# Performance work log

Measured on AMD Instinct MI355X. Metric: run time of the kernel, lower is better.

The kernel has to match this reference:

```python
import jax, jax.numpy as jnp
import numpy as np

N = 131072; E = 1048576; B = 1024
FIN = 128; H = 128; K = 30; C1 = 16; KERN = 5
D = 3 * H                      # 384 = hidden*num_layers
POOL_LEN = (K - KERN + 1) // 2 # 13
EPS = 1e-5


def setup_inputs() -> dict:
    key = jax.random.key(0)
    ks = jax.random.split(key, 12)
    w = lambda k, shape, s=0.05: (jax.random.normal(k, shape, jnp.float32) * s)
    z = jax.random.randint(ks[0], (N,), 0, FIN, dtype=jnp.int32)
    edge_index = jax.random.randint(ks[1], (2, E), 0, N, dtype=jnp.int32)
    batch = jnp.sort(jax.random.randint(ks[2], (N,), 0, B, dtype=jnp.int32))
    return dict(
        z=z, edge_index=edge_index, batch=batch,
        W0=w(ks[3], (FIN, H)), b0=jnp.zeros((H,), jnp.float32),
        W1=w(ks[4], (H, H)),   b1=jnp.zeros((H,), jnp.float32),
        W2=w(ks[5], (H, H)),   b2=jnp.zeros((H,), jnp.float32),
        Wc1=w(ks[6], (C1, D)), bc1=jnp.zeros((C1,), jnp.float32),
        Wc2=w(ks[7], (2 * C1, C1, KERN)), bc2=jnp.zeros((2 * C1,), jnp.float32),
        g1=jnp.ones((C1,), jnp.float32),  be1=jnp.zeros((C1,), jnp.float32),
        g2=jnp.ones((2 * C1,), jnp.float32), be2=jnp.zeros((2 * C1,), jnp.float32),
        Wl1=w(ks[8], (128, 2 * C1 * POOL_LEN)), bl1=jnp.zeros((128,), jnp.float32),
        Wl2=w(ks[9], (1, 128)), bl2=jnp.zeros((1,), jnp.float32),
        rm1=jnp.zeros((C1,), jnp.float32), rv1=jnp.ones((C1,), jnp.float32),
        rm2=jnp.zeros((2 * C1,), jnp.float32), rv2=jnp.ones((2 * C1,), jnp.float32),
    )


def _bn(h, g, be, rm, rv):
    # eval-mode BatchNorm1d over channel axis 1 of [B, C, L]
    scale = (g * jax.lax.rsqrt(rv + EPS))[None, :, None]
    return (h - rm[None, :, None]) * scale + be[None, :, None]


def _forward(z, edge_index, batch, W0, b0, W1, b1, W2, b2, Wc1, bc1, Wc2, bc2,
             g1, be1, g2, be2, Wl1, bl1, Wl2, bl2, rm1, rv1, rm2, rv2):
    # --- GCN normalization with self-loops (PyG gcn_norm) ---
    loops = jnp.arange(N)
    row = jnp.concatenate([edge_index[0], loops])  # source
    col = jnp.concatenate([edge_index[1], loops])  # target (aggregation)
    deg = jax.ops.segment_sum(jnp.ones(E + N, jnp.float32), col, num_segments=N)
    dis = jax.lax.rsqrt(deg)  # deg >= 1 thanks to self-loops
    norm = dis[row] * dis[col]

    def gcn(x, W, b):
        msg = (x @ W)[row] * norm[:, None]              # [E+N, H]
        return jax.ops.segment_sum(msg, col, num_segments=N) + b

    x = jax.nn.one_hot(z, FIN, dtype=jnp.float32)       # [N, FIN]
    xs = []
    for W, b in ((W0, b0), (W1, b1), (W2, b2)):
        x = jnp.tanh(gcn(x, W, b))
        xs.append(x)
    x = jnp.concatenate(xs, axis=-1)                    # [N, D]

    # --- global_sort_pool: per graph, sort by last channel desc, keep top-k, zero-pad ---
    order = jnp.lexsort((-x[:, -1], batch))             # batch asc, last-channel desc
    xb, bs = x[order], batch[order]
    counts = jax.ops.segment_sum(jnp.ones(N, jnp.int32), batch, num_segments=B)
    starts = jnp.cumsum(counts) - counts
    rank = jnp.arange(N) - starts[bs]                   # within-graph rank
    dest = jnp.where(rank < K, rank, K)                 # overflow bucket at K
    pooled = jnp.zeros((B, K + 1, D), jnp.float32).at[bs, dest].set(xb)[:, :K]  # [B,K,D]

    # --- conv1d_1 (kernel=stride=D) == dense over the D channels of each kept node ---
    h = jnp.einsum('bkd,cd->bck', pooled, Wc1) + bc1[None, :, None]  # [B,C1,K]
    h = _bn(jax.nn.relu(h), g1, be1, rm1, rv1)
    # --- conv1d_2 ---
    h = jax.lax.conv_general_dilated(h, Wc2, (1,), 'VALID',
                                     dimension_numbers=('NCH', 'OIH', 'NCH'))
    h = h + bc2[None, :, None]                          # [B,2C1,K-KERN+1]
    h = _bn(jax.nn.relu(h), g2, be2, rm2, rv2)
    # --- maxpool(2,2), flatten, dense head (dropout is identity in eval) ---
    h = h.reshape(B, 2 * C1, POOL_LEN, 2).max(-1)
    h = jax.nn.relu(h.reshape(B, -1) @ Wl1.T + bl1)
    return (h @ Wl2.T + bl2).reshape(-1)                # [B]


def reference(z, edge_index, batch, W0, b0, W1, b1, W2, b2, Wc1, bc1, Wc2, bc2,
              g1, be1, g2, be2, Wl1, bl1, Wl2, bl2, rm1, rv1, rm2, rv2):
    return _forward(z, edge_index, batch, W0, b0, W1, b1, W2, b2, Wc1, bc1, Wc2, bc2,
                    g1, be1, g2, be2, Wl1, bl1, Wl2, bl2, rm1, rv1, rm2, rv2)
```

## Files before the change

kernel.cpp:

```cpp
#include <hip/hip_runtime.h>
#include <math.h>

constexpr int HD = 128;
constexpr int DD = 384;
constexpr int KK = 30;
constexpr int C1N = 16;
constexpr int C2N = 32;
constexpr int KERN5 = 5;
constexpr int CONVL = 26;
constexpr int PL = 13;
constexpr int FLAT = 416;

__global__ void deg_kernel(const int* __restrict__ col, int* __restrict__ cnt, int E) {
  int e = blockIdx.x * blockDim.x + threadIdx.x;
  if (e < E) atomicAdd(&cnt[col[e]], 1);
}

__global__ void scan1_kernel(const int* __restrict__ cnt, int* __restrict__ bsum, int N) {
  __shared__ int red[256];
  int t = threadIdx.x, b = blockIdx.x;
  int base = b * 1024 + t * 4;
  int s = 0;
#pragma unroll
  for (int j = 0; j < 4; ++j) { int idx = base + j; if (idx < N) s += cnt[idx]; }
  red[t] = s;
  __syncthreads();
  for (int o = 128; o > 0; o >>= 1) { if (t < o) red[t] += red[t + o]; __syncthreads(); }
  if (t == 0) bsum[b] = red[0];
}

__global__ void scan2_kernel(int* __restrict__ bsum, int nb) {
  __shared__ int s[1024];
  int t = threadIdx.x;
  int v = (t < nb) ? bsum[t] : 0;
  s[t] = v;
  __syncthreads();
  for (int o = 1; o < 1024; o <<= 1) {
    int u = (t >= o) ? s[t - o] : 0;
    __syncthreads();
    s[t] += u;
    __syncthreads();
  }
  if (t < nb) bsum[t] = s[t] - v;
}

__global__ void scan3_kernel(const int* __restrict__ cnt, const int* __restrict__ bsum,
                             int* __restrict__ offsets, int N) {
  __shared__ int red[256];
  int t = threadIdx.x, b = blockIdx.x;
  int base = b * 1024 + t * 4;
  int v[4]; int s = 0;
#pragma unroll
  for (int j = 0; j < 4; ++j) { int idx = base + j; v[j] = (idx < N) ? cnt[idx] : 0; s += v[j]; }
  red[t] = s;
  __syncthreads();
  for (int o = 1; o < 256; o <<= 1) {
    int u = (t >= o) ? red[t - o] : 0;
    __syncthreads();
    red[t] += u;
    __syncthreads();
  }
  int run = bsum[b] + red[t] - s;
#pragma unroll
  for (int j = 0; j < 4; ++j) {
    int idx = base + j;
    if (idx < N) {
      offsets[idx] = run;
      run += v[j];
      if (idx == N - 1) offsets[N] = run;
    }
  }
}

__global__ void dis_kernel(const int* __restrict__ cnt, float* __restrict__ dis, int N) {
  int i = blockIdx.x * blockDim.x + threadIdx.x;
  if (i < N) dis[i] = 1.0f / sqrtf((float)(cnt[i] + 1));
}

__global__ void fill_kernel(const int* __restrict__ row, const int* __restrict__ col,
                            const int* __restrict__ offsets, int* __restrict__ cursor,
                            int* __restrict__ csr_src, int E) {
  int e = blockIdx.x * blockDim.x + threadIdx.x;
  if (e < E) {
    int c = col[e];
    int p = offsets[c] + atomicAdd(&cursor[c], 1);
    csr_src[p] = row[e];
  }
}

__global__ __launch_bounds__(256) void agg0_kernel(
    const int* __restrict__ z, const int* __restrict__ offsets,
    const int* __restrict__ csr_src, const float* __restrict__ dis,
    const float* __restrict__ W0, const float* __restrict__ b0,
    float* __restrict__ x1, int N) {
  int wid = (blockIdx.x * blockDim.x + threadIdx.x) >> 6;
  int lane = threadIdx.x & 63;
  if (wid >= N) return;
  int i = wid;
  int c0 = lane * 2;
  float di = dis[i];
  int beg = offsets[i], end = offsets[i + 1];
  float ax = 0.f, ay = 0.f;
  int e = beg;
  for (; e + 8 <= end; e += 8) {
    int s0 = csr_src[e],     s1 = csr_src[e + 1], s2 = csr_src[e + 2], s3 = csr_src[e + 3];
    int s4 = csr_src[e + 4], s5 = csr_src[e + 5], s6 = csr_src[e + 6], s7 = csr_src[e + 7];
    float w0 = dis[s0], w1 = dis[s1], w2 = dis[s2], w3 = dis[s3];
    float w4 = dis[s4], w5 = dis[s5], w6 = dis[s6], w7 = dis[s7];
    const float2 y0 = *(const float2*)(W0 + (size_t)z[s0] * HD + c0);
    const float2 y1 = *(const float2*)(W0 + (size_t)z[s1] * HD + c0);
    const float2 y2 = *(const float2*)(W0 + (size_t)z[s2] * HD + c0);
    const float2 y3 = *(const float2*)(W0 + (size_t)z[s3] * HD + c0);
    const float2 y4 = *(const float2*)(W0 + (size_t)z[s4] * HD + c0);
    const float2 y5 = *(const float2*)(W0 + (size_t)z[s5] * HD + c0);
    const float2 y6 = *(const float2*)(W0 + (size_t)z[s6] * HD + c0);
    const float2 y7 = *(const float2*)(W0 + (size_t)z[s7] * HD + c0);
    float axa = fmaf(w0, y0.x, fmaf(w1, y1.x, fmaf(w2, y2.x, w3 * y3.x)));
    float axb = fmaf(w4, y4.x, fmaf(w5, y5.x, fmaf(w6, y6.x, w7 * y7.x)));
    float aya = fmaf(w0, y0.y, fmaf(w1, y1.y, fmaf(w2, y2.y, w3 * y3.y)));
    float ayb = fmaf(w4, y4.y, fmaf(w5, y5.y, fmaf(w6, y6.y, w7 * y7.y)));
    ax += axa + axb;
    ay += aya + ayb;
  }
  for (; e + 4 <= end; e += 4) {
    int s0 = csr_src[e], s1 = csr_src[e + 1], s2 = csr_src[e + 2], s3 = csr_src[e + 3];
    float w0 = dis[s0], w1 = dis[s1], w2 = dis[s2], w3 = dis[s3];
    const float2 y0 = *(const float2*)(W0 + (size_t)z[s0] * HD + c0);
    const float2 y1 = *(const float2*)(W0 + (size_t)z[s1] * HD + c0);
    const float2 y2 = *(const float2*)(W0 + (size_t)z[s2] * HD + c0);
    const float2 y3 = *(const float2*)(W0 + (size_t)z[s3] * HD + c0);
    ax = fmaf(w0, y0.x, fmaf(w1, y1.x, fmaf(w2, y2.x, fmaf(w3, y3.x, ax))));
    ay = fmaf(w0, y0.y, fmaf(w1, y1.y, fmaf(w2, y2.y, fmaf(w3, y3.y, ay))));
  }
  for (; e < end; ++e) {
    int s = csr_src[e];
    float w = dis[s];
    const float2 ys = *(const float2*)(W0 + (size_t)z[s] * HD + c0);
    ax = fmaf(w, ys.x, ax);
    ay = fmaf(w, ys.y, ay);
  }
  const float2 yi = *(const float2*)(W0 + (size_t)z[i] * HD + c0);
  float inv = di * di;
  float ox = tanhf(di * ax + inv * yi.x + b0[c0]);
  float oy = tanhf(di * ay + inv * yi.y + b0[c0 + 1]);
  *(float2*)(x1 + (size_t)i * HD + c0) = make_float2(ox, oy);
}

__global__ __launch_bounds__(256) void agg_kernel(
    const float* __restrict__ x, const int* __restrict__ offsets,
    const int* __restrict__ csr_src, const float* __restrict__ dis,
    float* __restrict__ T, int N) {
  int wid = (blockIdx.x * blockDim.x + threadIdx.x) >> 6;
  int lane = threadIdx.x & 63;
  if (wid >= N) return;
  int i = wid;
  int c0 = lane * 2;
  float di = dis[i];
  int beg = offsets[i], end = offsets[i + 1];
  float ax = 0.f, ay = 0.f;
  int e = beg;
  for (; e + 8 <= end; e += 8) {
    int s0 = csr_src[e],     s1 = csr_src[e + 1], s2 = csr_src[e + 2], s3 = csr_src[e + 3];
    int s4 = csr_src[e + 4], s5 = csr_src[e + 5], s6 = csr_src[e + 6], s7 = csr_src[e + 7];
    float w0 = dis[s0], w1 = dis[s1], w2 = dis[s2], w3 = dis[s3];
    float w4 = dis[s4], w5 = dis[s5], w6 = dis[s6], w7 = dis[s7];
    const float2 y0 = *(const float2*)(x + (size_t)s0 * HD + c0);
    const float2 y1 = *(const float2*)(x + (size_t)s1 * HD + c0);
    const float2 y2 = *(const float2*)(x + (size_t)s2 * HD + c0);
    const float2 y3 = *(const float2*)(x + (size_t)s3 * HD + c0);
    const float2 y4 = *(const float2*)(x + (size_t)s4 * HD + c0);
    const float2 y5 = *(const float2*)(x + (size_t)s5 * HD + c0);
    const float2 y6 = *(const float2*)(x + (size_t)s6 * HD + c0);
    const float2 y7 = *(const float2*)(x + (size_t)s7 * HD + c0);
    float axa = fmaf(w0, y0.x, fmaf(w1, y1.x, fmaf(w2, y2.x, w3 * y3.x)));
    float axb = fmaf(w4, y4.x, fmaf(w5, y5.x, fmaf(w6, y6.x, w7 * y7.x)));
    float aya = fmaf(w0, y0.y, fmaf(w1, y1.y, fmaf(w2, y2.y, w3 * y3.y)));
    float ayb = fmaf(w4, y4.y, fmaf(w5, y5.y, fmaf(w6, y6.y, w7 * y7.y)));
    ax += axa + axb;
    ay += aya + ayb;
  }
  for (; e + 4 <= end; e += 4) {
    int s0 = csr_src[e], s1 = csr_src[e + 1], s2 = csr_src[e + 2], s3 = csr_src[e + 3];
    float w0 = dis[s0], w1 = dis[s1], w2 = dis[s2], w3 = dis[s3];
    const float2 y0 = *(const float2*)(x + (size_t)s0 * HD + c0);
    const float2 y1 = *(const float2*)(x + (size_t)s1 * HD + c0);
    const float2 y2 = *(const float2*)(x + (size_t)s2 * HD + c0);
    const float2 y3 = *(const float2*)(x + (size_t)s3 * HD + c0);
    ax = fmaf(w0, y0.x, fmaf(w1, y1.x, fmaf(w2, y2.x, fmaf(w3, y3.x, ax))));
    ay = fmaf(w0, y0.y, fmaf(w1, y1.y, fmaf(w2, y2.y, fmaf(w3, y3.y, ay))));
  }
  for (; e < end; ++e) {
    int s = csr_src[e];
    float w = dis[s];
    const float2 xs = *(const float2*)(x + (size_t)s * HD + c0);
    ax = fmaf(w, xs.x, ax);
    ay = fmaf(w, xs.y, ay);
  }
  const float2 xi = *(const float2*)(x + (size_t)i * HD + c0);
  float inv = di * di;
  float ox = di * ax + inv * xi.x;
  float oy = di * ay + inv * xi.y;
  *(float2*)(T + (size_t)i * HD + c0) = make_float2(ox, oy);
}

__global__ __launch_bounds__(256) void gemm_kernel(
    float* __restrict__ T, const float* __restrict__ W, const float* __restrict__ b, int N) {
  __shared__ float Xs[128][33];
  __shared__ float Ws[32][128];
  int t = threadIdx.x;
  int r0 = blockIdx.x * 128;
  int ty = t >> 4, tx = t & 15;
  int R0 = ty * 8;
  float acc[8][8];
#pragma unroll
  for (int a = 0; a < 8; ++a)
#pragma unroll
    for (int c = 0; c < 8; ++c) acc[a][c] = 0.f;

  for (int kb = 0; kb < 128; kb += 32) {
    __syncthreads();
    for (int l = t; l < 1024; l += 256) {
      int r = l >> 3, c4 = (l & 7) << 2;
      float4 v = *(const float4*)(T + (size_t)(r0 + r) * HD + kb + c4);
      Xs[r][c4] = v.x; Xs[r][c4 + 1] = v.y; Xs[r][c4 + 2] = v.z; Xs[r][c4 + 3] = v.w;
    }
    for (int l = t; l < 1024; l += 256) {
      int k = l >> 5, c4 = (l & 31) << 2;
      *(float4*)(&Ws[k][c4]) = *(const float4*)(W + (size_t)(kb + k) * HD + c4);
    }
    __syncthreads();
#pragma unroll
    for (int k = 0; k < 32; ++k) {
      float a[8];
#pragma unroll
      for (int ri = 0; ri < 8; ++ri) a[ri] = Xs[R0 + ri][k];
      float4 blo = *(const float4*)(&Ws[k][tx * 4]);
      float4 bhi = *(const float4*)(&Ws[k][64 + tx * 4]);
      float bb[8] = {blo.x, blo.y, blo.z, blo.w, bhi.x, bhi.y, bhi.z, bhi.w};
#pragma unroll
      for (int ri = 0; ri < 8; ++ri)
#pragma unroll
        for (int ci = 0; ci < 8; ++ci)
          acc[ri][ci] = fmaf(a[ri], bb[ci], acc[ri][ci]);
    }
  }
  float4 bl = *(const float4*)(b + tx * 4);
  float4 bh = *(const float4*)(b + 64 + tx * 4);
#pragma unroll
  for (int ri = 0; ri < 8; ++ri) {
    float4 o0 = make_float4(tanhf(acc[ri][0] + bl.x), tanhf(acc[ri][1] + bl.y),
                            tanhf(acc[ri][2] + bl.z), tanhf(acc[ri][3] + bl.w));
    float4 o1 = make_float4(tanhf(acc[ri][4] + bh.x), tanhf(acc[ri][5] + bh.y),
                            tanhf(acc[ri][6] + bh.z), tanhf(acc[ri][7] + bh.w));
    *(float4*)(T + (size_t)(r0 + R0 + ri) * HD + tx * 4) = o0;
    *(float4*)(T + (size_t)(r0 + R0 + ri) * HD + 64 + tx * 4) = o1;
  }
}

__global__ void gstart_kernel(const int* __restrict__ batch, int* __restrict__ gstart,
                              int N, int B) {
  int g = blockIdx.x * blockDim.x + threadIdx.x;
  if (g > B) return;
  int lo = 0, hi = N;
  while (lo < hi) { int mid = (lo + hi) >> 1; if (batch[mid] < g) lo = mid + 1; else hi = mid; }
  gstart[g] = lo;
}

__global__ __launch_bounds__(512) void head_kernel(
    const float* __restrict__ X1, const float* __restrict__ X2, const float* __restrict__ X3,
    const int* __restrict__ gstart,
    const float* __restrict__ Wc1, const float* __restrict__ bc1,
    const float* __restrict__ Wc2, const float* __restrict__ bc2,
    const float* __restrict__ g1, const float* __restrict__ be1,
    const float* __restrict__ g2, const float* __restrict__ be2,
    const float* __restrict__ rm1, const float* __restrict__ rv1,
    const float* __restrict__ rm2, const float* __restrict__ rv2,
    const float* __restrict__ Wl1, const float* __restrict__ bl1,
    const float* __restrict__ Wl2, const float* __restrict__ bl2,
    float* __restrict__ out) {
  constexpr int MAXC = 512;
  __shared__ float vals[MAXC];
  __shared__ int   sel[KK];
  __shared__ float ph[KK][385];
  __shared__ float h1b[C1N][KK + 1];
  float* h2b  = &ph[0][0];
  float* pp   = &ph[0][0] + 832;
  float* part = &ph[0][0] + 1248;
  float* l1v  = &ph[0][0] + 1760;

  int g = blockIdx.x, t = threadIdx.x;
  int start = gstart[g];
  int count = gstart[g + 1] - start;
  if (count > MAXC) count = MAXC;
  int kk = count < KK ? count : KK;

  for (int i = t; i < count; i += 512)
    vals[i] = X3[(size_t)(start + i) * HD + (HD - 1)];
  __syncthreads();
  if (t < count) {
    float vi = vals[t];
    int rank = 0;
    for (int j = 0; j < count; ++j) {
      float vj = vals[j];
      rank += (vj > vi) || (vj == vi && j < t);
    }
    if (rank < KK) sel[rank] = t;
  }
  __syncthreads();

  for (int l = t; l < KK * DD; l += 512) {
    int r = l / DD, d = l - r * DD;
    float v = 0.f;
    if (r < kk) {
      size_t n = (size_t)(start + sel[r]);
      v = (d < HD) ? X1[n * HD + d]
        : (d < 2 * HD) ? X2[n * HD + (d - HD)]
                       : X3[n * HD + (d - 2 * HD)];
    }
    ph[r][d] = v;
  }
  __syncthreads();

  if (t < C1N * KK) {
    int c = t / KK, k = t - c * KK;
    const float* w = Wc1 + c * DD;
    float s = bc1[c];
    for (int d = 0; d < DD; ++d) s = fmaf(ph[k][d], w[d], s);
    s = fmaxf(s, 0.f);
    float sc = g1[c] * rsqrtf(rv1[c] + 1e-5f);
    h1b[c][k] = (s - rm1[c]) * sc + be1[c];
  }
  __syncthreads();

  for (int l = t; l < C2N * CONVL; l += 512) {
    int o = l / CONVL, tt = l - o * CONVL;
    float s = bc2[o];
    const float* w = Wc2 + o * (C1N * KERN5);
#pragma unroll
    for (int c = 0; c < C1N; ++c)
#pragma unroll
      for (int q = 0; q < KERN5; ++q)
        s = fmaf(h1b[c][tt + q], w[c * KERN5 + q], s);
    s = fmaxf(s, 0.f);
    float sc = g2[o] * rsqrtf(rv2[o] + 1e-5f);
    h2b[o * CONVL + tt] = (s - rm2[o]) * sc + be2[o];
  }
  __syncthreads();

  if (t < FLAT) {
    int o = t / PL, u = t - o * PL;
    pp[t] = fmaxf(h2b[o * CONVL + 2 * u], h2b[o * CONVL + 2 * u + 1]);
  }
  __syncthreads();

  {
    int j = t & 127, h = t >> 7;
    const int Q = FLAT / 4;
    const float* w = Wl1 + (size_t)j * FLAT + h * Q;
    float s = (h == 0) ? bl1[j] : 0.f;
    for (int f = 0; f < Q; ++f) s = fmaf(pp[h * Q + f], w[f], s);
    part[t] = s;
  }
  __syncthreads();
  if (t < 128) l1v[t] = fmaxf(part[t] + part[t + 128] + part[t + 256] + part[t + 384], 0.f);
  __syncthreads();

  if (t < 64) {
    float s = l1v[t] * Wl2[t] + l1v[t + 64] * Wl2[t + 64];
#pragma unroll
    for (int o2 = 32; o2 > 0; o2 >>= 1) s += __shfl_down(s, o2);
    if (t == 0) out[g] = s + bl2[0];
  }
}

extern "C" void kernel_launch(void* const* d_in, const int* in_sizes, int n_in,
                              void* d_out, int out_size, void* d_ws, size_t ws_size,
                              hipStream_t stream) {
  const int*   z    = (const int*)d_in[0];
  const int*   ei   = (const int*)d_in[1];
  const int*   batch= (const int*)d_in[2];
  const float* W0   = (const float*)d_in[3];
  const float* b0   = (const float*)d_in[4];
  const float* W1   = (const float*)d_in[5];
  const float* b1   = (const float*)d_in[6];
  const float* W2   = (const float*)d_in[7];
  const float* b2   = (const float*)d_in[8];
  const float* Wc1  = (const float*)d_in[9];
  const float* bc1  = (const float*)d_in[10];
  const float* Wc2  = (const float*)d_in[11];
  const float* bc2  = (const float*)d_in[12];
  const float* g1   = (const float*)d_in[13];
  const float* be1  = (const float*)d_in[14];
  const float* g2   = (const float*)d_in[15];
  const float* be2  = (const float*)d_in[16];
  const float* Wl1  = (const float*)d_in[17];
  const float* bl1  = (const float*)d_in[18];
  const float* Wl2  = (const float*)d_in[19];
  const float* bl2  = (const float*)d_in[20];
  const float* rm1  = (const float*)d_in[21];
  const float* rv1  = (const float*)d_in[22];
  const float* rm2  = (const float*)d_in[23];
  const float* rv2  = (const float*)d_in[24];

  const int N = in_sizes[0];
  const int E = in_sizes[1] / 2;
  const int B = out_size;
  const int* rowp = ei;
  const int* colp = ei + E;

  char* base = (char*)d_ws;
  size_t off = 0;
  auto alloc = [&](size_t bytes) -> void* {
    void* p = base + off;
    off += (bytes + 255) & ~(size_t)255;
    return p;
  };
  int*   cnt     = (int*)alloc((size_t)N * 4);
  int*   offsets = (int*)alloc(((size_t)N + 1) * 4);
  int*   cursor  = (int*)alloc((size_t)N * 4);
  int*   csr_src = (int*)alloc((size_t)E * 4);
  float* dis     = (float*)alloc((size_t)N * 4);
  int*   gstart  = (int*)alloc(((size_t)B + 1) * 4);
  int*   bsum    = (int*)alloc(1024 * 4);
  float* X1      = (float*)alloc((size_t)N * HD * 4);
  float* X2      = (float*)alloc((size_t)N * HD * 4);
  float* X3      = (float*)alloc((size_t)N * HD * 4);
  (void)ws_size; (void)n_in;

  hipMemsetAsync(cnt, 0, (size_t)N * 4, stream);
  hipMemsetAsync(cursor, 0, (size_t)N * 4, stream);

  const int nb = (N + 1023) / 1024;
  deg_kernel<<<(E + 255) / 256, 256, 0, stream>>>(colp, cnt, E);
  scan1_kernel<<<nb, 256, 0, stream>>>(cnt, bsum, N);
  scan2_kernel<<<1, 1024, 0, stream>>>(bsum, nb);
  scan3_kernel<<<nb, 256, 0, stream>>>(cnt, bsum, offsets, N);
  dis_kernel<<<(N + 255) / 256, 256, 0, stream>>>(cnt, dis, N);
  fill_kernel<<<(E + 255) / 256, 256, 0, stream>>>(rowp, colp, offsets, cursor, csr_src, E);

  agg0_kernel<<<(N + 3) / 4, 256, 0, stream>>>(z, offsets, csr_src, dis, W0, b0, X1, N);
  agg_kernel<<<(N + 3) / 4, 256, 0, stream>>>(X1, offsets, csr_src, dis, X2, N);
  gemm_kernel<<<N / 128, 256, 0, stream>>>(X2, W1, b1, N);
  agg_kernel<<<(N + 3) / 4, 256, 0, stream>>>(X2, offsets, csr_src, dis, X3, N);
  gemm_kernel<<<N / 128, 256, 0, stream>>>(X3, W2, b2, N);

  gstart_kernel<<<(B + 1 + 255) / 256, 256, 0, stream>>>(batch, gstart, N, B);
  head_kernel<<<B, 512, 0, stream>>>(X1, X2, X3, gstart, Wc1, bc1, Wc2, bc2, g1, be1, g2, be2,
                                     rm1, rv1, rm2, rv2, Wl1, bl1, Wl2, bl2, (float*)d_out);
}
```

Before: 732.3 us.

## Fuse neighbor aggregation with dense transform in one layer kernel

Merges the aggregation kernel and the GEMM+tanh kernel into a single kernel per GCN layer. Each block aggregates 64 nodes into shared memory, then multiplies that tile by W and applies bias and tanh. This removes the global write and reread of the intermediate aggregated features and one launch per layer. The cost is larger shared memory (64x129 floats plus the W tile), a smaller GEMM tile of 4x8 per thread, and serialized aggregation of 16 nodes per wave, which may lower occupancy and latency hiding for the gathers.

```diff
diff --git a/kernel.cpp b/kernel.cpp
--- a/kernel.cpp
+++ b/kernel.cpp
@@ -146,84 +146,78 @@
   *(float2*)(x1 + (size_t)i * HD + c0) = make_float2(ox, oy);
 }
 
-__global__ __launch_bounds__(256) void agg_kernel(
+__global__ __launch_bounds__(256) void fused_layer_kernel(
     const float* __restrict__ x, const int* __restrict__ offsets,
     const int* __restrict__ csr_src, const float* __restrict__ dis,
-    float* __restrict__ T, int N) {
-  int wid = (blockIdx.x * blockDim.x + threadIdx.x) >> 6;
-  int lane = threadIdx.x & 63;
-  if (wid >= N) return;
-  int i = wid;
-  int c0 = lane * 2;
-  float di = dis[i];
-  int beg = offsets[i], end = offsets[i + 1];
-  float ax = 0.f, ay = 0.f;
-  int e = beg;
-  for (; e + 8 <= end; e += 8) {
-    int s0 = csr_src[e],     s1 = csr_src[e + 1], s2 = csr_src[e + 2], s3 = csr_src[e + 3];
-    int s4 = csr_src[e + 4], s5 = csr_src[e + 5], s6 = csr_src[e + 6], s7 = csr_src[e + 7];
-    float w0 = dis[s0], w1 = dis[s1], w2 = dis[s2], w3 = dis[s3];
-    float w4 = dis[s4], w5 = dis[s5], w6 = dis[s6], w7 = dis[s7];
-    const float2 y0 = *(const float2*)(x + (size_t)s0 * HD + c0);
-    const float2 y1 = *(const float2*)(x + (size_t)s1 * HD + c0);
-    const float2 y2 = *(const float2*)(x + (size_t)s2 * HD + c0);
-    const float2 y3 = *(const float2*)(x + (size_t)s3 * HD + c0);
-    const float2 y4 = *(const float2*)(x + (size_t)s4 * HD + c0);
-    const float2 y5 = *(const float2*)(x + (size_t)s5 * HD + c0);
-    const float2 y6 = *(const float2*)(x + (size_t)s6 * HD + c0);
-    const float2 y7 = *(const float2*)(x + (size_t)s7 * HD + c0);
-    float axa = fmaf(w0, y0.x, fmaf(w1, y1.x, fmaf(w2, y2.x, w3 * y3.x)));
-    float axb = fmaf(w4, y4.x, fmaf(w5, y5.x, fmaf(w6, y6.x, w7 * y7.x)));
-    float aya = fmaf(w0, y0.y, fmaf(w1, y1.y, fmaf(w2, y2.y, w3 * y3.y)));
-    float ayb = fmaf(w4, y4.y, fmaf(w5, y5.y, fmaf(w6, y6.y, w7 * y7.y)));
-    ax += axa + axb;
-    ay += aya + ayb;
-  }
-  for (; e + 4 <= end; e += 4) {
-    int s0 = csr_src[e], s1 = csr_src[e + 1], s2 = csr_src[e + 2], s3 = csr_src[e + 3];
-    float w0 = dis[s0], w1 = dis[s1], w2 = dis[s2], w3 = dis[s3];
-    const float2 y0 = *(const float2*)(x + (size_t)s0 * HD + c0);
-    const float2 y1 = *(const float2*)(x + (size_t)s1 * HD + c0);
-    const float2 y2 = *(const float2*)(x + (size_t)s2 * HD + c0);
-    const float2 y3 = *(const float2*)(x + (size_t)s3 * HD + c0);
-    ax = fmaf(w0, y0.x, fmaf(w1, y1.x, fmaf(w2, y2.x, fmaf(w3, y3.x, ax))));
-    ay = fmaf(w0, y0.y, fmaf(w1, y1.y, fmaf(w2, y2.y, fmaf(w3, y3.y, ay))));
-  }
-  for (; e < end; ++e) {
-    int s = csr_src[e];
-    float w = dis[s];
-    const float2 xs = *(const float2*)(x + (size_t)s * HD + c0);
-    ax = fmaf(w, xs.x, ax);
-    ay = fmaf(w, xs.y, ay);
-  }
-  const float2 xi = *(const float2*)(x + (size_t)i * HD + c0);
-  float inv = di * di;
-  float ox = di * ax + inv * xi.x;
-  float oy = di * ay + inv * xi.y;
-  *(float2*)(T + (size_t)i * HD + c0) = make_float2(ox, oy);
-}
-
-__global__ __launch_bounds__(256) void gemm_kernel(
-    float* __restrict__ T, const float* __restrict__ W, const float* __restrict__ b, int N) {
-  __shared__ float Xs[128][33];
+    const float* __restrict__ W, const float* __restrict__ b,
+    float* __restrict__ xout, int N) {
+  __shared__ float Xs[64][129];
   __shared__ float Ws[32][128];
   int t = threadIdx.x;
-  int r0 = blockIdx.x * 128;
+  int r0 = blockIdx.x * 64;
+  int w = t >> 6, lane = t & 63;
+  int c0 = lane * 2;
+
+  for (int it = 0; it < 16; ++it) {
+    int li = w * 16 + it;
+    int i = r0 + li;
+    float di = dis[i];
+    int beg = offsets[i], end = offsets[i + 1];
+    float ax = 0.f, ay = 0.f;
+    int e = beg;
+    for (; e + 8 <= end; e += 8) {
+      int s0 = csr_src[e],     s1 = csr_src[e + 1], s2 = csr_src[e + 2], s3 = csr_src[e + 3];
+      int s4 = csr_src[e + 4], s5 = csr_src[e + 5], s6 = csr_src[e + 6], s7 = csr_src[e + 7];
+      float w0 = dis[s0], w1 = dis[s1], w2 = dis[s2], w3 = dis[s3];
+      float w4 = dis[s4], w5 = dis[s5], w6 = dis[s6], w7 = dis[s7];
+      const float2 y0 = *(const float2*)(x + (size_t)s0 * HD + c0);
+      const float2 y1 = *(const float2*)(x + (size_t)s1 * HD + c0);
+      const float2 y2 = *(const float2*)(x + (size_t)s2 * HD + c0);
+      const float2 y3 = *(const float2*)(x + (size_t)s3 * HD + c0);
+      const float2 y4 = *(const float2*)(x + (size_t)s4 * HD + c0);
+      const float2 y5 = *(const float2*)(x + (size_t)s5 * HD + c0);
+      const float2 y6 = *(const float2*)(x + (size_t)s6 * HD + c0);
+      const float2 y7 = *(const float2*)(x + (size_t)s7 * HD + c0);
+      float axa = fmaf(w0, y0.x, fmaf(w1, y1.x, fmaf(w2, y2.x, w3 * y3.x)));
+      float axb = fmaf(w4, y4.x, fmaf(w5, y5.x, fmaf(w6, y6.x, w7 * y7.x)));
+      float aya = fmaf(w0, y0.y, fmaf(w1, y1.y, fmaf(w2, y2.y, w3 * y3.y)));
+      float ayb = fmaf(w4, y4.y, fmaf(w5, y5.y, fmaf(w6, y6.y, w7 * y7.y)));
+      ax += axa + axb;
+      ay += aya + ayb;
+    }
+    for (; e + 4 <= end; e += 4) {
+      int s0 = csr_src[e], s1 = csr_src[e + 1], s2 = csr_src[e + 2], s3 = csr_src[e + 3];
+      float w0 = dis[s0], w1 = dis[s1], w2 = dis[s2], w3 = dis[s3];
+      const float2 y0 = *(const float2*)(x + (size_t)s0 * HD + c0);
+      const float2 y1 = *(const float2*)(x + (size_t)s1 * HD + c0);
+      const float2 y2 = *(const float2*)(x + (size_t)s2 * HD + c0);
+      const float2 y3 = *(const float2*)(x + (size_t)s3 * HD + c0);
+      ax = fmaf(w0, y0.x, fmaf(w1, y1.x, fmaf(w2, y2.x, fmaf(w3, y3.x, ax))));
+      ay = fmaf(w0, y0.y, fmaf(w1, y1.y, fmaf(w2, y2.y, fmaf(w3, y3.y, ay))));
+    }
+    for (; e < end; ++e) {
+      int s = csr_src[e];
+      float ww = dis[s];
+      const float2 xs = *(const float2*)(x + (size_t)s * HD + c0);
+      ax = fmaf(ww, xs.x, ax);
+      ay = fmaf(ww, xs.y, ay);
+    }
+    const float2 xi = *(const float2*)(x + (size_t)i * HD + c0);
+    float inv = di * di;
+    Xs[li][c0]     = di * ax + inv * xi.x;
+    Xs[li][c0 + 1] = di * ay + inv * xi.y;
+  }
+
   int ty = t >> 4, tx = t & 15;
-  int R0 = ty * 8;
-  float acc[8][8];
-#pragma unroll
-  for (int a = 0; a < 8; ++a)
+  int R0 = ty * 4;
+  float acc[4][8];
+#pragma unroll
+  for (int a = 0; a < 4; ++a)
 #pragma unroll
     for (int c = 0; c < 8; ++c) acc[a][c] = 0.f;
 
   for (int kb = 0; kb < 128; kb += 32) {
     __syncthreads();
-    for (int l = t; l < 1024; l += 256) {
-      int r = l >> 3, c4 = (l & 7) << 2;
-      float4 v = *(const float4*)(T + (size_t)(r0 + r) * HD + kb + c4);
-      Xs[r][c4] = v.x; Xs[r][c4 + 1] = v.y; Xs[r][c4 + 2] = v.z; Xs[r][c4 + 3] = v.w;
-    }
     for (int l = t; l < 1024; l += 256) {
       int k = l >> 5, c4 = (l & 31) << 2;
       *(float4*)(&Ws[k][c4]) = *(const float4*)(W + (size_t)(kb + k) * HD + c4);
@@ -231,29 +225,31 @@
     __syncthreads();
 #pragma unroll
     for (int k = 0; k < 32; ++k) {
-      float a[8];
-#pragma unroll
-      for (int ri = 0; ri < 8; ++ri) a[ri] = Xs[R0 + ri][k];
+      float a0 = Xs[R0 + 0][kb + k];
+      float a1 = Xs[R0 + 1][kb + k];
+      float a2 = Xs[R0 + 2][kb + k];
+      float a3 = Xs[R0 + 3][kb + k];
       float4 blo = *(const float4*)(&Ws[k][tx * 4]);
       float4 bhi = *(const float4*)(&Ws[k][64 + tx * 4]);
       float bb[8] = {blo.x, blo.y, blo.z, blo.w, bhi.x, bhi.y, bhi.z, bhi.w};
-#pragma unroll
-      for (int ri = 0; ri < 8; ++ri)
+      float aa[4] = {a0, a1, a2, a3};
+#pragma unroll
+      for (int ri = 0; ri < 4; ++ri)
 #pragma unroll
         for (int ci = 0; ci < 8; ++ci)
-          acc[ri][ci] = fmaf(a[ri], bb[ci], acc[ri][ci]);
+          acc[ri][ci] = fmaf(aa[ri], bb[ci], acc[ri][ci]);
     }
   }
   float4 bl = *(const float4*)(b + tx * 4);
   float4 bh = *(const float4*)(b + 64 + tx * 4);
 #pragma unroll
-  for (int ri = 0; ri < 8; ++ri) {
+  for (int ri = 0; ri < 4; ++ri) {
     float4 o0 = make_float4(tanhf(acc[ri][0] + bl.x), tanhf(acc[ri][1] + bl.y),
                             tanhf(acc[ri][2] + bl.z), tanhf(acc[ri][3] + bl.w));
     float4 o1 = make_float4(tanhf(acc[ri][4] + bh.x), tanhf(acc[ri][5] + bh.y),
                             tanhf(acc[ri][6] + bh.z), tanhf(acc[ri][7] + bh.w));
-    *(float4*)(T + (size_t)(r0 + R0 + ri) * HD + tx * 4) = o0;
-    *(float4*)(T + (size_t)(r0 + R0 + ri) * HD + 64 + tx * 4) = o1;
+    *(float4*)(xout + (size_t)(r0 + R0 + ri) * HD + tx * 4) = o0;
+    *(float4*)(xout + (size_t)(r0 + R0 + ri) * HD + 64 + tx * 4) = o1;
   }
 }
 
@@ -439,10 +435,8 @@
   fill_kernel<<<(E + 255) / 256, 256, 0, stream>>>(rowp, colp, offsets, cursor, csr_src, E);
 
   agg0_kernel<<<(N + 3) / 4, 256, 0, stream>>>(z, offsets, csr_src, dis, W0, b0, X1, N);
-  agg_kernel<<<(N + 3) / 4, 256, 0, stream>>>(X1, offsets, csr_src, dis, X2, N);
-  gemm_kernel<<<N / 128, 256, 0, stream>>>(X2, W1, b1, N);
-  agg_kernel<<<(N + 3) / 4, 256, 0, stream>>>(X2, offsets, csr_src, dis, X3, N);
-  gemm_kernel<<<N / 128, 256, 0, stream>>>(X3, W2, b2, N);
+  fused_layer_kernel<<<N / 64, 256, 0, stream>>>(X1, offsets, csr_src, dis, W1, b1, X2, N);
+  fused_layer_kernel<<<N / 64, 256, 0, stream>>>(X2, offsets, csr_src, dis, W2, b2, X3, N);
 
   gstart_kernel<<<(B + 1 + 255) / 256, 256, 0, stream>>>(batch, gstart, N, B);
   head_kernel<<<B, 512, 0, stream>>>(X1, X2, X3, gstart, Wc1, bc1, Wc2, bc2, g1, be1, g2, be2,
```

After: 843.7 us. +15.2%, slower.
